# Performance work log

Measured on AMD Instinct MI355X. Metric: run time of the kernel, lower is better.

## Reference

```python
import jax, jax.numpy as jnp
import numpy as np

D_EMBED = 1024
D_CROSS = 768
N_HEADS = 16
D_HEAD = D_EMBED // N_HEADS


def setup_inputs() -> dict:
    key = jax.random.key(0)
    ks = jax.random.split(key, 10)
    s = 0.02
    return {
        "x": jax.random.normal(ks[0], (4, 4096, D_EMBED), dtype=jnp.float32),
        "y": jax.random.normal(ks[1], (4, 1024, D_CROSS), dtype=jnp.float32),
        "Wq": jax.random.normal(ks[2], (D_EMBED, D_EMBED), dtype=jnp.float32) * s,
        "bq": jnp.zeros((D_EMBED,), dtype=jnp.float32),
        "Wk": jax.random.normal(ks[3], (D_CROSS, D_EMBED), dtype=jnp.float32) * s,
        "bk": jnp.zeros((D_EMBED,), dtype=jnp.float32),
        "Wv": jax.random.normal(ks[4], (D_CROSS, D_EMBED), dtype=jnp.float32) * s,
        "bv": jnp.zeros((D_EMBED,), dtype=jnp.float32),
        "Wo": jax.random.normal(ks[5], (D_EMBED, D_EMBED), dtype=jnp.float32) * s,
        "bo": jnp.zeros((D_EMBED,), dtype=jnp.float32),
    }


def reference(x, y, Wq, bq, Wk, bk, Wv, bv, Wo, bo):
    b, sq, _ = x.shape
    skv = y.shape[1]
    # projections
    q = x @ Wq + bq   # [b, sq, d_embed]
    k = y @ Wk + bk   # [b, skv, d_embed]
    v = y @ Wv + bv   # [b, skv, d_embed]
    # split heads: [b, h, s, d_head]
    q = q.reshape(b, sq, N_HEADS, D_HEAD).transpose(0, 2, 1, 3)
    k = k.reshape(b, skv, N_HEADS, D_HEAD).transpose(0, 2, 1, 3)
    v = v.reshape(b, skv, N_HEADS, D_HEAD).transpose(0, 2, 1, 3)
    scale = 1.0 / jnp.sqrt(jnp.float32(D_HEAD))
    scores = jnp.einsum("bhqd,bhkd->bhqk", q, k) * scale
    attn = jax.nn.softmax(scores, axis=-1)
    out = jnp.einsum("bhqk,bhkd->bhqd", attn, v)
    out = out.transpose(0, 2, 1, 3).reshape(b, sq, D_EMBED)
    return out @ Wo + bo
```

## Files before the change

kernel.cpp:

```cpp
#include <hip/hip_runtime.h>

typedef unsigned short ushort_t;
typedef __attribute__((ext_vector_type(8))) __bf16 bf16x8;
typedef __attribute__((ext_vector_type(4))) float floatx4;
typedef __attribute__((ext_vector_type(8))) unsigned short ushortx8;
typedef __attribute__((ext_vector_type(4))) unsigned short ushortx4;
typedef __attribute__((ext_vector_type(4))) short short4v;
typedef __attribute__((ext_vector_type(2))) unsigned uint2v;

__device__ __forceinline__ ushort_t f2bf(float f) {
    union { float f; unsigned u; } v; v.f = f;
    unsigned r = v.u + 0x7fffu + ((v.u >> 16) & 1u);
    return (ushort_t)(r >> 16);
}

__device__ __forceinline__ void gld_lds16(const ushort_t* g, ushort_t* l) {
    __builtin_amdgcn_global_load_lds(
        (const __attribute__((address_space(1))) unsigned*)g,
        (__attribute__((address_space(3))) unsigned*)l, 16, 0, 0);
}

__device__ __forceinline__ unsigned pk_bf16(float a, float b) {
    unsigned ua = __builtin_bit_cast(unsigned, a) + 0x8000u;
    unsigned ub = __builtin_bit_cast(unsigned, b) + 0x8000u;
    return __builtin_amdgcn_perm(ub, ua, 0x07060302u);
}

__global__ __launch_bounds__(256) void prep(
    const float* __restrict__ x, const float* __restrict__ y,
    const float* __restrict__ Wq, const float* __restrict__ Wo,
    const float* __restrict__ Wk, const float* __restrict__ Wv,
    ushort_t* __restrict__ xb, ushort_t* __restrict__ yb,
    ushort_t* __restrict__ Wqt, ushort_t* __restrict__ Wot,
    ushort_t* __restrict__ Wkvt) {
    const int bid = blockIdx.x;
    if (bid < 19456) {
        const int NX = 4194304;
        int i = bid * 256 + threadIdx.x;
        float4 v; ushortx4* dst;
        if (i < NX) { v = ((const float4*)x)[i]; dst = (ushortx4*)xb + i; }
        else        { int j = i - NX; v = ((const float4*)y)[j]; dst = (ushortx4*)yb + j; }
        ushortx4 o;
        o.x = f2bf(v.x); o.y = f2bf(v.y); o.z = f2bf(v.z); o.w = f2bf(v.w);
        *dst = o;
        return;
    }
    __shared__ ushort_t t[32][33];
    const float* W; ushort_t* Wt; int K, n0, k0;
    if (bid < 21504) {
        int tt = bid - 19456;
        W = (tt >> 10) ? Wo : Wq;
        Wt = (tt >> 10) ? Wot : Wqt;
        K = 1024;
        int r = tt & 1023;
        n0 = (r & 31) * 32; k0 = (r >> 5) * 32;
    } else {
        int tt = bid - 21504;
        int z = tt / 768, r = tt - z * 768;
        W = z ? Wv : Wk;
        Wt = Wkvt + (size_t)z * 786432;
        K = 768;
        n0 = (r & 31) * 32; k0 = (r >> 5) * 32;
    }
    const int tx = threadIdx.x & 31, ty = threadIdx.x >> 5;
#pragma unroll
    for (int i = 0; i < 4; ++i)
        t[ty + 8 * i][tx] = f2bf(W[(size_t)(k0 + ty + 8 * i) * 1024 + n0 + tx]);
    __syncthreads();
#pragma unroll
    for (int i = 0; i < 4; ++i)
        Wt[(size_t)(n0 + ty + 8 * i) * K + k0 + tx] = t[tx][ty + 8 * i];
}

__device__ __forceinline__ void gemm_core(
    const ushort_t* __restrict__ A, const ushort_t* __restrict__ Bt,
    int K, int m0, int n0, ushort_t* As, ushort_t* Bs,
    floatx4 (&acc)[4][4], int tid, int wr, int wc, int quad, int l16) {
    const ushort_t* ga0 = A + (size_t)(m0 + (tid >> 2)) * K + (tid & 3) * 8;
    const ushort_t* ga1 = A + (size_t)(m0 + 64 + (tid >> 2)) * K + (tid & 3) * 8;
    const ushort_t* gb0 = Bt + (size_t)(n0 + (tid >> 2)) * K + (tid & 3) * 8;
    const ushort_t* gb1 = Bt + (size_t)(n0 + 64 + (tid >> 2)) * K + (tid & 3) * 8;
    ushort_t* la0 = As + tid * 8;
    ushort_t* la1 = As + (tid + 256) * 8;
    ushort_t* lb0 = Bs + tid * 8;
    ushort_t* lb1 = Bs + (tid + 256) * 8;

    for (int kt = 0; kt < K; kt += 32) {
        __syncthreads();
        gld_lds16(ga0, la0); gld_lds16(ga1, la1);
        gld_lds16(gb0, lb0); gld_lds16(gb1, lb1);
        ga0 += 32; ga1 += 32; gb0 += 32; gb1 += 32;
        __syncthreads();
        bf16x8 af[4], bfr[4];
#pragma unroll
        for (int i = 0; i < 4; ++i)
            af[i] = *(const bf16x8*)(As + (wr * 64 + i * 16 + l16) * 32 + quad * 8);
#pragma unroll
        for (int j = 0; j < 4; ++j)
            bfr[j] = *(const bf16x8*)(Bs + (wc * 64 + j * 16 + l16) * 32 + quad * 8);
#pragma unroll
        for (int i = 0; i < 4; ++i)
#pragma unroll
            for (int j = 0; j < 4; ++j)
                acc[i][j] = __builtin_amdgcn_mfma_f32_16x16x32_bf16(af[i], bfr[j], acc[i][j], 0, 0, 0);
    }
}

__global__ __launch_bounds__(256) void proj_kv(
    const ushort_t* __restrict__ yb, const ushort_t* __restrict__ Wkvt,
    const float* __restrict__ bk, const float* __restrict__ bv,
    ushort_t* __restrict__ Kc, ushort_t* __restrict__ Vc) {
    __shared__ __align__(16) ushort_t As[128 * 32];
    __shared__ __align__(16) ushort_t Bs[128 * 32];
    const int tid = threadIdx.x;
    const int lane = tid & 63, w = tid >> 6;
    const int quad = lane >> 4, l16 = lane & 15;
    const int wr = w >> 1, wc = w & 1;
    const int id2 = blockIdx.x;
    const int m0 = (id2 & 31) * 128, n0 = (id2 >> 5) * 128;
    floatx4 acc[4][4] = {};
    gemm_core(yb, Wkvt, 768, m0, n0, As, Bs, acc, tid, wr, wc, quad, l16);
    if (n0 < 1024) {
#pragma unroll
        for (int i = 0; i < 4; ++i) {
            const int rowb = m0 + wr * 64 + i * 16 + quad * 4;
            const int b = rowb >> 10, kvt = (rowb & 1023) >> 6, kvr = rowb & 63;
#pragma unroll
            for (int j = 0; j < 4; ++j) {
                const int col = n0 + wc * 64 + j * 16 + l16;
                const int h = col >> 6, d = col & 63;
                const float bval = bk[col];
                ushort_t* base = Kc + (((size_t)b * 16 + h) * 16 + kvt) * 4096 +
                                 (d >> 3) * 512 + kvr * 8 + (d & 7);
#pragma unroll
                for (int r = 0; r < 4; ++r)
                    base[r * 8] = f2bf(acc[i][j][r] + bval);
            }
        }
    } else {
#pragma unroll
        for (int i = 0; i < 4; ++i) {
            const int rowb = m0 + wr * 64 + i * 16 + quad * 4;
            const int b = rowb >> 10, kvt = (rowb & 1023) >> 6, sub = (rowb >> 3) & 7;
#pragma unroll
            for (int j = 0; j < 4; ++j) {
                const int col = n0 + wc * 64 + j * 16 + l16;
                const int nc = col - 1024;
                const int h = nc >> 6, d = nc & 63;
                const float bval = bv[nc];
                ushortx4 o;
#pragma unroll
                for (int r = 0; r < 4; ++r) o[r] = f2bf(acc[i][j][r] + bval);
                *(ushortx4*)(Vc + (((size_t)b * 16 + h) * 16 + kvt) * 4096 +
                             sub * 512 + d * 8 + (quad & 1) * 4) = o;
            }
        }
    }
}

__device__ __forceinline__ void gemm256_core(
    const ushort_t* __restrict__ A, const ushort_t* __restrict__ Bt,
    ushort_t* lds, floatx4 (&acc)[8][4],
    int m0, int n0, int tid, int wr, int wc, int quad, int l16) {
    const int K = 1024, NT = 32;
    const int cx = (quad ^ (l16 & 3)) * 8;

    const int ra = tid >> 2;
    const int ka = (tid & 3) ^ (ra & 3);
    const ushort_t* gA0 = A + (size_t)(m0 + ra) * K + ka * 8;
    const ushort_t* gA1 = gA0 + (size_t)128 * K;
    const ushort_t* gB0 = Bt + (size_t)(n0 + ra) * K + ka * 8;
    const ushort_t* gB1 = gB0 + (size_t)128 * K;
    const int dA0 = tid * 8, dA1 = tid * 8 + 4096;
    const int dB0 = 8192 + tid * 8, dB1 = 8192 + tid * 8 + 4096;

#pragma unroll
    for (int pt = 0; pt < 2; ++pt) {
        ushort_t* d = lds + pt * 16384;
        gld_lds16(gA0, d + dA0); gld_lds16(gA1, d + dA1);
        gld_lds16(gB0, d + dB0); gld_lds16(gB1, d + dB1);
        gA0 += 32; gA1 += 32; gB0 += 32; gB1 += 32;
    }

    int cur = 0, nxt = 2;
    for (int t = 0; t < NT; ++t) {
        if (t < NT - 1) asm volatile("s_waitcnt vmcnt(4)" ::: "memory");
        else            asm volatile("s_waitcnt vmcnt(0)" ::: "memory");
        __builtin_amdgcn_s_barrier();
        __builtin_amdgcn_sched_barrier(0);
        const ushort_t* Abase = lds + cur * 16384;
        const ushort_t* Bbase = Abase + 8192;
        ushort_t* dn = lds + nxt * 16384;

        bf16x8 af[4], bfr[4];
#pragma unroll
        for (int fr = 0; fr < 4; ++fr)
            af[fr] = *(const bf16x8*)(Abase + (wr * 128 + fr * 16 + l16) * 32 + cx);
#pragma unroll
        for (int fc = 0; fc < 4; ++fc)
            bfr[fc] = *(const bf16x8*)(Bbase + (wc * 64 + fc * 16 + l16) * 32 + cx);
        if (t + 2 < NT) { gld_lds16(gA0, dn + dA0); gld_lds16(gA1, dn + dA1); }
        asm volatile("s_waitcnt lgkmcnt(0)" ::: "memory");
        __builtin_amdgcn_sched_barrier(0);
        __builtin_amdgcn_s_setprio(1);
#pragma unroll
        for (int fr = 0; fr < 4; ++fr)
#pragma unroll
            for (int fc = 0; fc < 4; ++fc)
                acc[fr][fc] = __builtin_amdgcn_mfma_f32_16x16x32_bf16(af[fr], bfr[fc], acc[fr][fc], 0, 0, 0);
        __builtin_amdgcn_s_setprio(0);
        __builtin_amdgcn_sched_barrier(0);
        __builtin_amdgcn_s_barrier();
        __builtin_amdgcn_sched_barrier(0);

#pragma unroll
        for (int fr = 0; fr < 4; ++fr)
            af[fr] = *(const bf16x8*)(Abase + (wr * 128 + 64 + fr * 16 + l16) * 32 + cx);
        if (t + 2 < NT) {
            gld_lds16(gB0, dn + dB0); gld_lds16(gB1, dn + dB1);
            gA0 += 32; gA1 += 32; gB0 += 32; gB1 += 32;
        }
        asm volatile("s_waitcnt lgkmcnt(0)" ::: "memory");
        __builtin_amdgcn_sched_barrier(0);
        __builtin_amdgcn_s_setprio(1);
#pragma unroll
        for (int fr = 0; fr < 4; ++fr)
#pragma unroll
            for (int fc = 0; fc < 4; ++fc)
                acc[fr + 4][fc] = __builtin_amdgcn_mfma_f32_16x16x32_bf16(af[fr], bfr[fc], acc[fr + 4][fc], 0, 0, 0);
        __builtin_amdgcn_s_setprio(0);
        cur = cur == 2 ? 0 : cur + 1;
        nxt = nxt == 2 ? 0 : nxt + 1;
    }
}

__global__ __launch_bounds__(512, 2) void gemm256_q(
    const ushort_t* __restrict__ A, const ushort_t* __restrict__ Bt,
    const float* __restrict__ bq, ushort_t* __restrict__ Qc, float qscale) {
    __shared__ __align__(16) ushort_t lds[49152];
    const int tid = threadIdx.x;
    const int lane = tid & 63, w = tid >> 6;
    const int quad = lane >> 4, l16 = lane & 15;
    const int wr = w >> 2, wc = w & 3;
    const int bid = blockIdx.x;
    const int swz = (bid & 7) * 32 + (bid >> 3);
    const int m0 = (swz >> 2) * 256, n0 = (swz & 3) * 256;

    floatx4 acc[8][4] = {};
    gemm256_core(A, Bt, lds, acc, m0, n0, tid, wr, wc, quad, l16);

#pragma unroll
    for (int fr = 0; fr < 8; ++fr) {
        const int rowb = m0 + wr * 128 + fr * 16 + quad * 4;
        const int b_ = rowb >> 12, q = rowb & 4095;
#pragma unroll
        for (int fc = 0; fc < 4; ++fc) {
            const int col = n0 + wc * 64 + fc * 16 + l16;
            const float bval = bq[col];
            const int h = col >> 6, d = col & 63;
            ushort_t* base = Qc +
                (((size_t)b_ * 16 + h) * 32 + (q >> 7)) * 8192 +
                (d >> 3) * 1024 + (size_t)(q & 127) * 8 + (d & 7);
#pragma unroll
            for (int r = 0; r < 4; ++r)
                base[r * 8] = f2bf((acc[fr][fc][r] + bval) * qscale);
        }
    }
}

__global__ __launch_bounds__(512, 2) void gemm256_o(
    const ushort_t* __restrict__ A, const ushort_t* __restrict__ Bt,
    const float* __restrict__ bias, float* __restrict__ C) {
    __shared__ __align__(16) ushort_t lds[49152];
    const int tid = threadIdx.x;
    const int lane = tid & 63, w = tid >> 6;
    const int quad = lane >> 4, l16 = lane & 15;
    const int wr = w >> 2, wc = w & 3;
    const int bid = blockIdx.x;
    const int swz = (bid & 7) * 32 + (bid >> 3);
    const int m0 = (swz >> 2) * 256, n0 = (swz & 3) * 256;

    floatx4 acc[8][4] = {};
    gemm256_core(A, Bt, lds, acc, m0, n0, tid, wr, wc, quad, l16);

#pragma unroll
    for (int fr = 0; fr < 8; ++fr) {
        const int rowb = m0 + wr * 128 + fr * 16 + quad * 4;
#pragma unroll
        for (int fc = 0; fc < 4; ++fc) {
            const int col = n0 + wc * 64 + fc * 16 + l16;
            const float bval = bias[col];
#pragma unroll
            for (int r = 0; r < 4; ++r)
                C[(size_t)(rowb + r) * 1024 + col] = acc[fr][fc][r] + bval;
        }
    }
}

__device__ __forceinline__ void stage_kv(const ushort_t* kg, const ushort_t* vg,
                                         ushort_t* dst, int tid) {
#pragma unroll
    for (int i = 0; i < 2; ++i) {
        int s = i * 256 + tid;
        gld_lds16(kg + s * 8, dst + s * 8);
        gld_lds16(vg + s * 8, dst + 4096 + s * 8);
    }
}

__global__ __launch_bounds__(256, 4) void attn_kernel(
    const ushort_t* __restrict__ Qc,
    const ushort_t* __restrict__ Kc,
    const ushort_t* __restrict__ Vc,
    ushort_t* __restrict__ O)
{
    __shared__ __align__(16) ushort_t smem[16384];
    const int tid = threadIdx.x;
    const int w = tid >> 6, lane = tid & 63;
    const int quad = lane >> 4, l16 = lane & 15;
    const int q0 = blockIdx.x * 128;
    const int bh = blockIdx.y, b = bh >> 4;

    const ushort_t* qg = Qc + ((size_t)bh * 32 + blockIdx.x) * 8192;
    bf16x8 qf[2][2];
#pragma unroll
    for (int ks = 0; ks < 2; ++ks)
#pragma unroll
        for (int qt = 0; qt < 2; ++qt)
            qf[ks][qt] = *(const bf16x8*)(qg +
                ((ks * 4 + quad) * 128 + w * 32 + qt * 16 + l16) * 8);

    const ushort_t* kvbase = Kc + (size_t)bh * 65536;
    const ushort_t* vvbase = Vc + (size_t)bh * 65536;
    stage_kv(kvbase, vvbase, smem, tid);
    __syncthreads();

    floatx4 oacc[4][2] = {};
    float lsum[2] = {0.f, 0.f};

    for (int kvt = 0; kvt < 16; ++kvt) {
        const int sel = kvt & 1;
        if (kvt < 15)
            stage_kv(kvbase + (kvt + 1) * 4096, vvbase + (kvt + 1) * 4096,
                     smem + (sel ^ 1) * 8192, tid);
        const ushort_t* pK = smem + sel * 8192;
        const ushort_t* pV = pK + 4096;

        floatx4 st[4][2] = {};
#pragma unroll
        for (int ks = 0; ks < 2; ++ks) {
            bf16x8 ak[4];
#pragma unroll
            for (int m4 = 0; m4 < 4; ++m4)
                ak[m4] = *(const bf16x8*)(pK + ((ks * 4 + quad) * 64 + m4 * 16 + l16) * 8);
#pragma unroll
            for (int m4 = 0; m4 < 4; ++m4)
#pragma unroll
                for (int qt = 0; qt < 2; ++qt)
                    st[m4][qt] = __builtin_amdgcn_mfma_f32_16x16x32_bf16(ak[m4], qf[ks][qt], st[m4][qt], 0, 0, 0);
        }

        uint2v pk[4][2];
#pragma unroll
        for (int qt = 0; qt < 2; ++qt) {
            float acc = 0.f;
#pragma unroll
            for (int m4 = 0; m4 < 4; ++m4) {
                float p0 = __builtin_amdgcn_exp2f(st[m4][qt][0]);
                float p1 = __builtin_amdgcn_exp2f(st[m4][qt][1]);
                float p2 = __builtin_amdgcn_exp2f(st[m4][qt][2]);
                float p3 = __builtin_amdgcn_exp2f(st[m4][qt][3]);
                acc += (p0 + p1) + (p2 + p3);
                pk[m4][qt].x = pk_bf16(p0, p1);
                pk[m4][qt].y = pk_bf16(p2, p3);
            }
            lsum[qt] += acc;
        }

#pragma unroll
        for (int m4 = 0; m4 < 4; ++m4) {
#pragma unroll
            for (int dt = 0; dt < 4; ++dt) {
                short4v av = *(const short4v*)(pV +
                    ((m4 * 2 + (quad >> 1)) * 64 + dt * 16 + l16) * 8 + (quad & 1) * 4);
#pragma unroll
                for (int qt = 0; qt < 2; ++qt) {
                    short4v bp = __builtin_bit_cast(short4v, pk[m4][qt]);
                    oacc[dt][qt] = __builtin_amdgcn_mfma_f32_16x16x16bf16_1k(av, bp, oacc[dt][qt], 0, 0, 0);
                }
            }
        }
        __syncthreads();
    }

    const int h = bh & 15;
    float inv[2];
#pragma unroll
    for (int qt = 0; qt < 2; ++qt) {
        float l = lsum[qt];
        l += __shfl_xor(l, 16, 64);
        l += __shfl_xor(l, 32, 64);
        inv[qt] = 1.0f / l;
    }
#pragma unroll
    for (int dt = 0; dt < 4; ++dt)
#pragma unroll
        for (int qt = 0; qt < 2; ++qt) {
            uint2v o2;
            o2.x = pk_bf16(oacc[dt][qt][0] * inv[qt], oacc[dt][qt][1] * inv[qt]);
            o2.y = pk_bf16(oacc[dt][qt][2] * inv[qt], oacc[dt][qt][3] * inv[qt]);
            *(uint2v*)(smem + (w * 32 + qt * 16 + l16) * 68 + dt * 16 + quad * 4) = o2;
        }
    __syncthreads();
#pragma unroll
    for (int i = 0; i < 8; ++i) {
        int s = i * 256 + tid;
        int row = s >> 4, dc = s & 15;
        ushortx4 v = *(const ushortx4*)(smem + row * 68 + dc * 4);
        *(ushortx4*)(O + (size_t)(b * 4096 + q0 + row) * 1024 + h * 64 + dc * 4) = v;
    }
}

extern "C" void kernel_launch(void* const* d_in, const int* in_sizes, int n_in,
                              void* d_out, int out_size, void* d_ws, size_t ws_size,
                              hipStream_t stream) {
    const float* x  = (const float*)d_in[0];
    const float* y  = (const float*)d_in[1];
    const float* Wq = (const float*)d_in[2];
    const float* bq = (const float*)d_in[3];
    const float* Wk = (const float*)d_in[4];
    const float* bk = (const float*)d_in[5];
    const float* Wv = (const float*)d_in[6];
    const float* bv = (const float*)d_in[7];
    const float* Wo = (const float*)d_in[8];
    const float* bo = (const float*)d_in[9];

    char* ws = (char*)d_ws;
    ushort_t* xb   = (ushort_t*)(ws);
    ushort_t* yb   = (ushort_t*)(ws + 33554432);
    ushort_t* Wqt  = (ushort_t*)(ws + 39845888);
    ushort_t* Wkvt = (ushort_t*)(ws + 41943040);
    ushort_t* Wot  = (ushort_t*)(ws + 45088768);
    ushort_t* Qc   = (ushort_t*)(ws + 47185920);
    ushort_t* Kc   = (ushort_t*)(ws + 80740352);
    ushort_t* Vc   = (ushort_t*)(ws + 89128960);
    ushort_t* Ab   = (ushort_t*)(ws + 97517568);

    const float QSCALE = 0.125f * 1.44269504f;

    prep<<<23040, 256, 0, stream>>>(x, y, Wq, Wo, Wk, Wv, xb, yb, Wqt, Wot, Wkvt);
    gemm256_q<<<256, 512, 0, stream>>>(xb, Wqt, bq, Qc, QSCALE);
    proj_kv<<<512, 256, 0, stream>>>(yb, Wkvt, bk, bv, Kc, Vc);
    attn_kernel<<<dim3(32, 64), 256, 0, stream>>>(Qc, Kc, Vc, Ab);
    gemm256_o<<<256, 512, 0, stream>>>(Ab, Wot, bo, (float*)d_out);
}
```

Before: 343.6 us.

## Merge Q and KV projections into one 256-tile launch and restructure GEMM pipeline

The separate Q projection and the 128-tile KV projection kernel are merged into a single launch of 384 blocks that share the pipelined 256x256 GEMM core. K and NT become parameters so the same core serves both. Inside the core, all four global-to-LDS prefetches are issued together, and the second half of the A fragments is loaded into a separate register set before the first MFMA batch, which removes the mid-iteration barrier. The LDS XOR swizzle is changed to a different bit pattern to reduce bank conflicts. The extra fragment registers may raise register pressure.

```diff
diff --git a/kernel.cpp b/kernel.cpp
--- a/kernel.cpp
+++ b/kernel.cpp
@@ -72,101 +72,14 @@
         Wt[(size_t)(n0 + ty + 8 * i) * K + k0 + tx] = t[tx][ty + 8 * i];
 }
 
-__device__ __forceinline__ void gemm_core(
-    const ushort_t* __restrict__ A, const ushort_t* __restrict__ Bt,
-    int K, int m0, int n0, ushort_t* As, ushort_t* Bs,
-    floatx4 (&acc)[4][4], int tid, int wr, int wc, int quad, int l16) {
-    const ushort_t* ga0 = A + (size_t)(m0 + (tid >> 2)) * K + (tid & 3) * 8;
-    const ushort_t* ga1 = A + (size_t)(m0 + 64 + (tid >> 2)) * K + (tid & 3) * 8;
-    const ushort_t* gb0 = Bt + (size_t)(n0 + (tid >> 2)) * K + (tid & 3) * 8;
-    const ushort_t* gb1 = Bt + (size_t)(n0 + 64 + (tid >> 2)) * K + (tid & 3) * 8;
-    ushort_t* la0 = As + tid * 8;
-    ushort_t* la1 = As + (tid + 256) * 8;
-    ushort_t* lb0 = Bs + tid * 8;
-    ushort_t* lb1 = Bs + (tid + 256) * 8;
-
-    for (int kt = 0; kt < K; kt += 32) {
-        __syncthreads();
-        gld_lds16(ga0, la0); gld_lds16(ga1, la1);
-        gld_lds16(gb0, lb0); gld_lds16(gb1, lb1);
-        ga0 += 32; ga1 += 32; gb0 += 32; gb1 += 32;
-        __syncthreads();
-        bf16x8 af[4], bfr[4];
-#pragma unroll
-        for (int i = 0; i < 4; ++i)
-            af[i] = *(const bf16x8*)(As + (wr * 64 + i * 16 + l16) * 32 + quad * 8);
-#pragma unroll
-        for (int j = 0; j < 4; ++j)
-            bfr[j] = *(const bf16x8*)(Bs + (wc * 64 + j * 16 + l16) * 32 + quad * 8);
-#pragma unroll
-        for (int i = 0; i < 4; ++i)
-#pragma unroll
-            for (int j = 0; j < 4; ++j)
-                acc[i][j] = __builtin_amdgcn_mfma_f32_16x16x32_bf16(af[i], bfr[j], acc[i][j], 0, 0, 0);
-    }
-}
-
-__global__ __launch_bounds__(256) void proj_kv(
-    const ushort_t* __restrict__ yb, const ushort_t* __restrict__ Wkvt,
-    const float* __restrict__ bk, const float* __restrict__ bv,
-    ushort_t* __restrict__ Kc, ushort_t* __restrict__ Vc) {
-    __shared__ __align__(16) ushort_t As[128 * 32];
-    __shared__ __align__(16) ushort_t Bs[128 * 32];
-    const int tid = threadIdx.x;
-    const int lane = tid & 63, w = tid >> 6;
-    const int quad = lane >> 4, l16 = lane & 15;
-    const int wr = w >> 1, wc = w & 1;
-    const int id2 = blockIdx.x;
-    const int m0 = (id2 & 31) * 128, n0 = (id2 >> 5) * 128;
-    floatx4 acc[4][4] = {};
-    gemm_core(yb, Wkvt, 768, m0, n0, As, Bs, acc, tid, wr, wc, quad, l16);
-    if (n0 < 1024) {
-#pragma unroll
-        for (int i = 0; i < 4; ++i) {
-            const int rowb = m0 + wr * 64 + i * 16 + quad * 4;
-            const int b = rowb >> 10, kvt = (rowb & 1023) >> 6, kvr = rowb & 63;
-#pragma unroll
-            for (int j = 0; j < 4; ++j) {
-                const int col = n0 + wc * 64 + j * 16 + l16;
-                const int h = col >> 6, d = col & 63;
-                const float bval = bk[col];
-                ushort_t* base = Kc + (((size_t)b * 16 + h) * 16 + kvt) * 4096 +
-                                 (d >> 3) * 512 + kvr * 8 + (d & 7);
-#pragma unroll
-                for (int r = 0; r < 4; ++r)
-                    base[r * 8] = f2bf(acc[i][j][r] + bval);
-            }
-        }
-    } else {
-#pragma unroll
-        for (int i = 0; i < 4; ++i) {
-            const int rowb = m0 + wr * 64 + i * 16 + quad * 4;
-            const int b = rowb >> 10, kvt = (rowb & 1023) >> 6, sub = (rowb >> 3) & 7;
-#pragma unroll
-            for (int j = 0; j < 4; ++j) {
-                const int col = n0 + wc * 64 + j * 16 + l16;
-                const int nc = col - 1024;
-                const int h = nc >> 6, d = nc & 63;
-                const float bval = bv[nc];
-                ushortx4 o;
-#pragma unroll
-                for (int r = 0; r < 4; ++r) o[r] = f2bf(acc[i][j][r] + bval);
-                *(ushortx4*)(Vc + (((size_t)b * 16 + h) * 16 + kvt) * 4096 +
-                             sub * 512 + d * 8 + (quad & 1) * 4) = o;
-            }
-        }
-    }
-}
-
 __device__ __forceinline__ void gemm256_core(
     const ushort_t* __restrict__ A, const ushort_t* __restrict__ Bt,
-    ushort_t* lds, floatx4 (&acc)[8][4],
+    int K, int NT, ushort_t* lds, floatx4 (&acc)[8][4],
     int m0, int n0, int tid, int wr, int wc, int quad, int l16) {
-    const int K = 1024, NT = 32;
-    const int cx = (quad ^ (l16 & 3)) * 8;
+    const int cx = (quad ^ ((l16 >> 1) & 3)) * 8;
 
     const int ra = tid >> 2;
-    const int ka = (tid & 3) ^ (ra & 3);
+    const int ka = (tid & 3) ^ ((tid >> 3) & 3);
     const ushort_t* gA0 = A + (size_t)(m0 + ra) * K + ka * 8;
     const ushort_t* gA1 = gA0 + (size_t)128 * K;
     const ushort_t* gB0 = Bt + (size_t)(n0 + ra) * K + ka * 8;
@@ -192,15 +105,24 @@
         const ushort_t* Bbase = Abase + 8192;
         ushort_t* dn = lds + nxt * 16384;
 
-        bf16x8 af[4], bfr[4];
+        bf16x8 af[4], bfr[4], af2[4];
 #pragma unroll
         for (int fr = 0; fr < 4; ++fr)
             af[fr] = *(const bf16x8*)(Abase + (wr * 128 + fr * 16 + l16) * 32 + cx);
 #pragma unroll
         for (int fc = 0; fc < 4; ++fc)
             bfr[fc] = *(const bf16x8*)(Bbase + (wc * 64 + fc * 16 + l16) * 32 + cx);
-        if (t + 2 < NT) { gld_lds16(gA0, dn + dA0); gld_lds16(gA1, dn + dA1); }
-        asm volatile("s_waitcnt lgkmcnt(0)" ::: "memory");
+        __builtin_amdgcn_sched_barrier(0);
+        if (t + 2 < NT) {
+            gld_lds16(gA0, dn + dA0); gld_lds16(gA1, dn + dA1);
+            gld_lds16(gB0, dn + dB0); gld_lds16(gB1, dn + dB1);
+            gA0 += 32; gA1 += 32; gB0 += 32; gB1 += 32;
+        }
+        __builtin_amdgcn_sched_barrier(0);
+#pragma unroll
+        for (int fr = 0; fr < 4; ++fr)
+            af2[fr] = *(const bf16x8*)(Abase + (wr * 128 + 64 + fr * 16 + l16) * 32 + cx);
+        asm volatile("s_waitcnt lgkmcnt(4)" ::: "memory");
         __builtin_amdgcn_sched_barrier(0);
         __builtin_amdgcn_s_setprio(1);
 #pragma unroll
@@ -209,61 +131,96 @@
             for (int fc = 0; fc < 4; ++fc)
                 acc[fr][fc] = __builtin_amdgcn_mfma_f32_16x16x32_bf16(af[fr], bfr[fc], acc[fr][fc], 0, 0, 0);
         __builtin_amdgcn_s_setprio(0);
-        __builtin_amdgcn_sched_barrier(0);
-        __builtin_amdgcn_s_barrier();
-        __builtin_amdgcn_sched_barrier(0);
-
+        asm volatile("s_waitcnt lgkmcnt(0)" ::: "memory");
+        __builtin_amdgcn_sched_barrier(0);
+        __builtin_amdgcn_s_setprio(1);
 #pragma unroll
         for (int fr = 0; fr < 4; ++fr)
-            af[fr] = *(const bf16x8*)(Abase + (wr * 128 + 64 + fr * 16 + l16) * 32 + cx);
-        if (t + 2 < NT) {
-            gld_lds16(gB0, dn + dB0); gld_lds16(gB1, dn + dB1);
-            gA0 += 32; gA1 += 32; gB0 += 32; gB1 += 32;
-        }
-        asm volatile("s_waitcnt lgkmcnt(0)" ::: "memory");
-        __builtin_amdgcn_sched_barrier(0);
-        __builtin_amdgcn_s_setprio(1);
-#pragma unroll
-        for (int fr = 0; fr < 4; ++fr)
 #pragma unroll
             for (int fc = 0; fc < 4; ++fc)
-                acc[fr + 4][fc] = __builtin_amdgcn_mfma_f32_16x16x32_bf16(af[fr], bfr[fc], acc[fr + 4][fc], 0, 0, 0);
+                acc[fr + 4][fc] = __builtin_amdgcn_mfma_f32_16x16x32_bf16(af2[fr], bfr[fc], acc[fr + 4][fc], 0, 0, 0);
         __builtin_amdgcn_s_setprio(0);
+        __builtin_amdgcn_sched_barrier(0);
         cur = cur == 2 ? 0 : cur + 1;
         nxt = nxt == 2 ? 0 : nxt + 1;
     }
 }
 
-__global__ __launch_bounds__(512, 2) void gemm256_q(
-    const ushort_t* __restrict__ A, const ushort_t* __restrict__ Bt,
-    const float* __restrict__ bq, ushort_t* __restrict__ Qc, float qscale) {
+__global__ __launch_bounds__(512, 2) void proj256(
+    const ushort_t* __restrict__ xb, const ushort_t* __restrict__ yb,
+    const ushort_t* __restrict__ Wqt, const ushort_t* __restrict__ Wkvt,
+    const float* __restrict__ bq, const float* __restrict__ bk, const float* __restrict__ bv,
+    ushort_t* __restrict__ Qc, ushort_t* __restrict__ Kc, ushort_t* __restrict__ Vc,
+    float qscale) {
     __shared__ __align__(16) ushort_t lds[49152];
     const int tid = threadIdx.x;
     const int lane = tid & 63, w = tid >> 6;
     const int quad = lane >> 4, l16 = lane & 15;
     const int wr = w >> 2, wc = w & 3;
     const int bid = blockIdx.x;
-    const int swz = (bid & 7) * 32 + (bid >> 3);
-    const int m0 = (swz >> 2) * 256, n0 = (swz & 3) * 256;
-
     floatx4 acc[8][4] = {};
-    gemm256_core(A, Bt, lds, acc, m0, n0, tid, wr, wc, quad, l16);
-
-#pragma unroll
-    for (int fr = 0; fr < 8; ++fr) {
-        const int rowb = m0 + wr * 128 + fr * 16 + quad * 4;
-        const int b_ = rowb >> 12, q = rowb & 4095;
-#pragma unroll
-        for (int fc = 0; fc < 4; ++fc) {
-            const int col = n0 + wc * 64 + fc * 16 + l16;
-            const float bval = bq[col];
-            const int h = col >> 6, d = col & 63;
-            ushort_t* base = Qc +
-                (((size_t)b_ * 16 + h) * 32 + (q >> 7)) * 8192 +
-                (d >> 3) * 1024 + (size_t)(q & 127) * 8 + (d & 7);
-#pragma unroll
-            for (int r = 0; r < 4; ++r)
-                base[r * 8] = f2bf((acc[fr][fc][r] + bval) * qscale);
+
+    if (bid < 256) {
+        const int swz = (bid & 7) * 32 + (bid >> 3);
+        const int m0 = (swz >> 2) * 256, n0 = (swz & 3) * 256;
+        gemm256_core(xb, Wqt, 1024, 32, lds, acc, m0, n0, tid, wr, wc, quad, l16);
+#pragma unroll
+        for (int fr = 0; fr < 8; ++fr) {
+            const int rowb = m0 + wr * 128 + fr * 16 + quad * 4;
+            const int b_ = rowb >> 12, q = rowb & 4095;
+#pragma unroll
+            for (int fc = 0; fc < 4; ++fc) {
+                const int col = n0 + wc * 64 + fc * 16 + l16;
+                const float bval = bq[col];
+                const int h = col >> 6, d = col & 63;
+                ushort_t* base = Qc +
+                    (((size_t)b_ * 16 + h) * 32 + (q >> 7)) * 8192 +
+                    (d >> 3) * 1024 + (size_t)(q & 127) * 8 + (d & 7);
+#pragma unroll
+                for (int r = 0; r < 4; ++r)
+                    base[r * 8] = f2bf((acc[fr][fc][r] + bval) * qscale);
+            }
+        }
+    } else {
+        const int id2 = bid - 256;
+        const int kvswz = (id2 & 7) * 16 + (id2 >> 3);
+        const int m0 = (kvswz >> 3) * 256, n0 = (kvswz & 7) * 256;
+        gemm256_core(yb, Wkvt, 768, 24, lds, acc, m0, n0, tid, wr, wc, quad, l16);
+        if (n0 < 1024) {
+#pragma unroll
+            for (int fr = 0; fr < 8; ++fr) {
+                const int rowb = m0 + wr * 128 + fr * 16 + quad * 4;
+                const int b = rowb >> 10, kvt = (rowb & 1023) >> 6, kvr = rowb & 63;
+#pragma unroll
+                for (int fc = 0; fc < 4; ++fc) {
+                    const int col = n0 + wc * 64 + fc * 16 + l16;
+                    const int h = col >> 6, d = col & 63;
+                    const float bval = bk[col];
+                    ushort_t* base = Kc + (((size_t)b * 16 + h) * 16 + kvt) * 4096 +
+                                     (d >> 3) * 512 + kvr * 8 + (d & 7);
+#pragma unroll
+                    for (int r = 0; r < 4; ++r)
+                        base[r * 8] = f2bf(acc[fr][fc][r] + bval);
+                }
+            }
+        } else {
+#pragma unroll
+            for (int fr = 0; fr < 8; ++fr) {
+                const int rowb = m0 + wr * 128 + fr * 16 + quad * 4;
+                const int b = rowb >> 10, kvt = (rowb & 1023) >> 6, sub = (rowb >> 3) & 7;
+#pragma unroll
+                for (int fc = 0; fc < 4; ++fc) {
+                    const int col = n0 + wc * 64 + fc * 16 + l16;
+                    const int nc = col - 1024;
+                    const int h = nc >> 6, d = nc & 63;
+                    const float bval = bv[nc];
+                    ushortx4 o;
+#pragma unroll
+                    for (int r = 0; r < 4; ++r) o[r] = f2bf(acc[fr][fc][r] + bval);
+                    *(ushortx4*)(Vc + (((size_t)b * 16 + h) * 16 + kvt) * 4096 +
+                                 sub * 512 + d * 8 + (quad & 1) * 4) = o;
+                }
+            }
         }
     }
 }
@@ -281,7 +238,7 @@
     const int m0 = (swz >> 2) * 256, n0 = (swz & 3) * 256;
 
     floatx4 acc[8][4] = {};
-    gemm256_core(A, Bt, lds, acc, m0, n0, tid, wr, wc, quad, l16);
+    gemm256_core(A, Bt, 1024, 32, lds, acc, m0, n0, tid, wr, wc, quad, l16);
 
 #pragma unroll
     for (int fr = 0; fr < 8; ++fr) {
@@ -448,8 +405,7 @@
     const float QSCALE = 0.125f * 1.44269504f;
 
     prep<<<23040, 256, 0, stream>>>(x, y, Wq, Wo, Wk, Wv, xb, yb, Wqt, Wot, Wkvt);
-    gemm256_q<<<256, 512, 0, stream>>>(xb, Wqt, bq, Qc, QSCALE);
-    proj_kv<<<512, 256, 0, stream>>>(yb, Wkvt, bk, bv, Kc, Vc);
+    proj256<<<384, 512, 0, stream>>>(xb, yb, Wqt, Wkvt, bq, bk, bv, Qc, Kc, Vc, QSCALE);
     attn_kernel<<<dim3(32, 64), 256, 0, stream>>>(Qc, Kc, Vc, Ab);
     gemm256_o<<<256, 512, 0, stream>>>(Ab, Wot, bo, (float*)d_out);
 }
```

Result: faster. 336.3 us (-2.1%).
